# Performance work log

Hardware: AMD Instinct MI355X
Metric: run time of the kernel (lower is better)

Reference implementation:

```python
import jax, jax.numpy as jnp
import numpy as np

NUM_CLASSES = 3
DICE_W, FOCAL_W, CONTR_W = 1.0, 1.0, 0.1
GAMMA, ALPHA = 2.0, 0.25
TEMP = 0.1
SCALE_WEIGHTS = (1.0, 0.8, 0.6)
SMOOTH = 1e-5


def setup_inputs() -> dict:
    key = jax.random.key(0)
    ks = jax.random.split(key, 7)
    return {
        "pred_maps": jax.random.normal(ks[0], (2, 3, 128, 128, 128), jnp.float32),
        "target": jax.random.randint(ks[1], (2, 128, 128, 128), 0, 3, jnp.int64),
        "fmap0": jax.random.normal(ks[2], (2, 48, 16, 16, 16), jnp.float32),
        "fmap1": jax.random.normal(ks[3], (2, 48, 8, 8, 8), jnp.float32),
        "fmap2": jax.random.normal(ks[4], (2, 48, 4, 4, 4), jnp.float32),
        "logits": jax.random.normal(ks[5], (2, 3), jnp.float32),
        "labels": jax.random.randint(ks[6], (2, 3), 0, 2, jnp.int32),
    }


def _dice_loss(pred, target):
    p = jax.nn.softmax(pred, axis=1)                      # [B,C,H,W,D]
    t = jnp.where(target == -1, 0, target)
    oh = jax.nn.one_hot(t, NUM_CLASSES, axis=1, dtype=p.dtype)  # [B,C,H,W,D]
    inter = (p * oh).sum((2, 3, 4))                       # [B,C]
    union = p.sum((2, 3, 4)) + oh.sum((2, 3, 4))
    dice = (2.0 * inter + SMOOTH) / (union + SMOOTH)      # [B,C]
    return 1.0 - dice[:, 1:].mean()                       # exclude background


def _focal_loss(logits, labels):
    pt = jax.nn.sigmoid(logits)
    pt = jnp.where(labels == 1, pt, 1.0 - pt)
    return (-ALPHA * (1.0 - pt) ** GAMMA * jnp.log(pt + 1e-6)).mean()


def _pair_loss(E, wa, wb, offdiag, positive):
    # E: [B,N,N] exp(sim/T); wa, wb: [B,N] class indicator weights
    W = wa[:, :, None] * wb[:, None, :]
    if offdiag is not None:
        W = W * offdiag
    cnt = W.sum((1, 2))
    mean = (E * W).sum((1, 2)) / jnp.maximum(cnt, 1.0)
    val = -jnp.log(mean + 1e-6) if positive else jnp.log1p(mean)
    return jnp.where(cnt > 0, val, 0.0)                   # [B]


def _scale_loss(feat, mask):
    B, C = feat.shape[:2]
    f = feat.reshape(B, C, -1)                            # [B,C,N]
    norm = jnp.sqrt((f * f).sum(1, keepdims=True))
    f = f / jnp.maximum(norm, 1e-12)                      # F.normalize(dim=1)
    m = mask.reshape(B, -1)                               # [B,N]
    E = jnp.exp(jnp.einsum('bcn,bcm->bnm', f, f) / TEMP)  # [B,N,N]
    N = m.shape[1]
    off = 1.0 - jnp.eye(N, dtype=f.dtype)
    w0 = (m == 0).astype(f.dtype)
    w1 = (m == 1).astype(f.dtype)
    w2 = (m == 2).astype(f.dtype)
    loss = _pair_loss(E, w1, w1, off, True)               # htx positive
    loss += _pair_loss(E, w2, w2, off, True)              # mh positive
    loss += _pair_loss(E, w1, w2, None, False)            # htx vs mh
    loss += _pair_loss(E, w0, w1, None, False)            # bg vs htx
    loss += _pair_loss(E, w0, w2, None, False)            # bg vs mh
    return loss.mean()                                    # batch_loss / B


def _contrastive_loss(fmaps, target):
    H = target.shape[1]
    total = 0.0
    for feat, w in zip(fmaps, SCALE_WEIGHTS):
        s = H // feat.shape[2]                            # exact nearest-downsample stride
        mask = target[:, ::s, ::s, ::s]
        total += w * _scale_loss(feat, mask)
    return total


def reference(pred_maps, target, fmap0, fmap1, fmap2, logits, labels):
    dice = _dice_loss(pred_maps, target)
    focal = _focal_loss(logits, labels)
    contr = _contrastive_loss((fmap0, fmap1, fmap2), target)
    total = DICE_W * dice + FOCAL_W * focal + CONTR_W * contr
    return (total, dice, focal, contr)
```

## Files before the change

kernel.cpp:

```cpp
#include <hip/hip_runtime.h>
#include <math.h>

#define VOX (128*128*128)
#define NCH 48

typedef _Float16 half8 __attribute__((ext_vector_type(8)));
typedef float floatx4 __attribute__((ext_vector_type(4)));

__device__ __forceinline__ float waveSum(float v) {
#pragma unroll
    for (int off = 32; off > 0; off >>= 1) v += __shfl_down(v, off, 64);
    return v;
}


__global__ void zero_ws(int* p) { p[threadIdx.x] = 0; }

__global__ __launch_bounds__(256) void count_kernel(const int* __restrict__ target,
                                                    int* __restrict__ cnt) {
    const int scale = blockIdx.y, b = blockIdx.z, z = scale * 2 + b;
    const int N    = (scale == 0) ? 4096 : (scale == 1) ? 512 : 64;
    const int Npad = (scale == 0) ? 4096 : (scale == 1) ? 512 : 128;
    const int n = blockIdx.x * blockDim.x + threadIdx.x;
    int myK = -1;
    if (n < N) {
        const int d = (scale == 0) ? 16 : (scale == 1) ? 8 : 4;
        const int s = 128 / d;
        int i3 = n % d, i2 = (n / d) % d, i1 = n / (d * d);
        myK = target[(size_t)b * VOX + (size_t)(i1 * s) * 16384 + (i2 * s) * 128 + (i3 * s)];
    } else if (n < Npad) {
        myK = 3;
    }
    const int lane = threadIdx.x & 63;
#pragma unroll
    for (int k = 0; k < 4; k++) {
        unsigned long long mb = __ballot(myK == k);
        if (mb && lane == (__ffsll((unsigned long long)mb) - 1))
            atomicAdd(&cnt[z * 4 + k], (int)__popcll(mb));
    }
}

__global__ __launch_bounds__(256) void dice_kernel(const float* __restrict__ pred,
                                                   const int* __restrict__ target,
                                                   float* __restrict__ dice_stage) {
    const int b = blockIdx.z;
    const float4* p0 = (const float4*)(pred + (size_t)b * 3 * VOX);
    const float4* p1 = (const float4*)(pred + (size_t)b * 3 * VOX + VOX);
    const float4* p2 = (const float4*)(pred + (size_t)b * 3 * VOX + 2 * VOX);
    const int4*   tg = (const int4*)(target + (size_t)b * VOX);

    float vals[6] = {0, 0, 0, 0, 0, 0};
    const int V4 = VOX / 4;
    const int stride = gridDim.x * blockDim.x;
    for (int v = blockIdx.x * blockDim.x + threadIdx.x; v < V4; v += stride) {
        float4 a = p0[v], bq = p1[v], cq = p2[v];
        int4 t = tg[v];
        float xs[4][3] = {{a.x, bq.x, cq.x}, {a.y, bq.y, cq.y},
                          {a.z, bq.z, cq.z}, {a.w, bq.w, cq.w}};
        int ts[4] = {t.x, t.y, t.z, t.w};
#pragma unroll
        for (int e = 0; e < 4; e++) {
            float e0 = __expf(xs[e][0]), e1 = __expf(xs[e][1]), e2 = __expf(xs[e][2]);
            float inv = 1.0f / (e0 + e1 + e2);
            float q1 = e1 * inv, q2 = e2 * inv;
            vals[2] += q1;
            vals[3] += q2;
            int tt = ts[e];
            vals[0] += (tt == 1) ? q1 : 0.0f;
            vals[1] += (tt == 2) ? q2 : 0.0f;
            vals[4] += (tt == 1) ? 1.0f : 0.0f;
            vals[5] += (tt == 2) ? 1.0f : 0.0f;
        }
    }
    __shared__ float red[4][6];
    int lane = threadIdx.x & 63, wid = threadIdx.x >> 6;
#pragma unroll
    for (int k = 0; k < 6; k++) {
        float s = waveSum(vals[k]);
        if (lane == 0) red[wid][k] = s;
    }
    __syncthreads();
    if (threadIdx.x < 6) {
        float s = red[0][threadIdx.x] + red[1][threadIdx.x] +
                  red[2][threadIdx.x] + red[3][threadIdx.x];
        dice_stage[(size_t)(b * 512 + blockIdx.x) * 8 + threadIdx.x] = s;
    }
}

__global__ __launch_bounds__(256) void norm_scatter(const float* __restrict__ f0in,
                                                    const float* __restrict__ f1in,
                                                    const float* __restrict__ f2in,
                                                    const int* __restrict__ target,
                                                    _Float16* __restrict__ Fh0,
                                                    _Float16* __restrict__ Fh1,
                                                    _Float16* __restrict__ Fh2,
                                                    const int* __restrict__ cnt,
                                                    int* __restrict__ cursor) {
    const int scale = blockIdx.y, b = blockIdx.z, z = scale * 2 + b;
    const int N    = (scale == 0) ? 4096 : (scale == 1) ? 512 : 64;
    const int Npad = (scale == 0) ? 4096 : (scale == 1) ? 512 : 128;
    const int n = blockIdx.x * blockDim.x + threadIdx.x;
    const int lane = threadIdx.x & 63;

    const int c0 = cnt[z * 4 + 0], c1 = cnt[z * 4 + 1], c2 = cnt[z * 4 + 2];
    const int bases[4] = {0, c0, c0 + c1, c0 + c1 + c2};

    int myK = -1;
    float v[NCH];
    float inv = 0.0f;
    if (n < N) {
        const float* fi = ((scale == 0) ? f0in : (scale == 1) ? f1in : f2in)
                          + (size_t)b * NCH * N + n;
        float ss = 0.0f;
#pragma unroll
        for (int c = 0; c < NCH; c++) { v[c] = fi[(size_t)c * N]; ss += v[c] * v[c]; }
        inv = 1.0f / fmaxf(sqrtf(ss), 1e-12f);
        const int d = (scale == 0) ? 16 : (scale == 1) ? 8 : 4;
        const int s = 128 / d;
        int i3 = n % d, i2 = (n / d) % d, i1 = n / (d * d);
        myK = target[(size_t)b * VOX + (size_t)(i1 * s) * 16384 + (i2 * s) * 128 + (i3 * s)];
    } else if (n < Npad) {
        myK = 3;
#pragma unroll
        for (int c = 0; c < NCH; c++) v[c] = 0.0f;
    }

    int dest = -1;
#pragma unroll
    for (int k = 0; k < 4; k++) {
        unsigned long long mb = __ballot(myK == k);
        int base = 0;
        if (mb) {
            int leader = __ffsll((unsigned long long)mb) - 1;
            if (lane == leader)
                base = atomicAdd(&cursor[z * 4 + k], (int)__popcll(mb));
            base = __shfl(base, leader, 64);
            if (myK == k) {
                int pos = (int)__popcll(mb & ((1ull << lane) - 1ull));
                dest = bases[k] + base + pos;
            }
        }
    }

    if (myK >= 0) {
        _Float16* fo = ((scale == 0) ? Fh0 : (scale == 1) ? Fh1 : Fh2)
                       + (size_t)b * Npad * 64 + (size_t)dest * 64;
#pragma unroll
        for (int g = 0; g < 8; g++) {
            half8 h;
#pragma unroll
            for (int e = 0; e < 8; e++) {
                int c = g * 8 + e;
                h[e] = (c < NCH) ? (_Float16)(v[c] * inv) : (_Float16)0.0f;
            }
            *(half8*)(fo + g * 8) = h;
        }
    }
}

__global__ __launch_bounds__(256) void pair_mfma(const _Float16* __restrict__ Fh0,
                                                 const _Float16* __restrict__ Fh1,
                                                 const _Float16* __restrict__ Fh2,
                                                 const int* __restrict__ cnt,
                                                 float* __restrict__ pair_stage) {
    const int bid = blockIdx.x;
    int z, t;
    if (bid < 1056)      { z = bid / 528; t = bid % 528; }
    else if (bid < 1076) { int i = bid - 1056; z = 2 + i / 10; t = i % 10; }
    else                 { z = 4 + (bid - 1076); t = 0; }

    const int scale = z >> 1, b = z & 1;
    const int Npad = (scale == 0) ? 4096 : (scale == 1) ? 512 : 128;
    const _Float16* F = ((scale == 0) ? Fh0 : (scale == 1) ? Fh1 : Fh2)
                        + (size_t)b * Npad * 64;
    const int B1 = cnt[z * 4 + 0];
    const int B2 = B1 + cnt[z * 4 + 1];
    const int B3 = B2 + cnt[z * 4 + 2];

    int by = (int)((sqrtf(8.0f * (float)t + 1.0f) - 1.0f) * 0.5f);
    while ((by + 1) * (by + 2) / 2 <= t) by++;
    while (by * (by + 1) / 2 > t) by--;
    int bx = t - by * (by + 1) / 2;

    const int tid = threadIdx.x, lane = tid & 63, w = tid >> 6;
    const int wi = w >> 1, wj = w & 1;
    const int m = lane & 15, q = lane >> 4;
    const int ib = bx * 128 + wi * 64, jb = by * 128 + wj * 64;

    float s[5] = {0, 0, 0, 0, 0};

    const bool diag = (ib == jb);
    const bool below = (ib > jb);
    int ciL = (ib >= B1) + (ib >= B2) + (ib >= B3);
    int ciH = (ib + 63 >= B1) + (ib + 63 >= B2) + (ib + 63 >= B3);
    int cjL = (jb >= B1) + (jb >= B2) + (jb >= B3);
    int cjH = (jb + 63 >= B1) + (jb + 63 >= B2) + (jb + 63 >= B3);
    const bool pure = (ciL == ciH) && (cjL == cjH) && !diag;
    int bucket = -1;
    float mult = 1.0f;
    if (pure) {
        int ci = ciL, cj = cjL;
        if (ci == 1 && cj == 1) { bucket = 0; mult = 2.0f; }
        else if (ci == 2 && cj == 2) { bucket = 1; mult = 2.0f; }
        else if (ci == 1 && cj == 2) bucket = 2;
        else if (ci == 0 && cj == 1) bucket = 3;
        else if (ci == 0 && cj == 2) bucket = 4;
    }
    const bool skip = below || (pure && bucket < 0);

    if (!skip) {
        const _Float16* Ai = F + (size_t)(ib + m) * 64 + q * 8;
        const _Float16* Bj = F + (size_t)(jb + m) * 64 + q * 8;

        floatx4 acc_[4][4] = {};
#pragma unroll
        for (int k = 0; k < 2; k++) {
            half8 aF[4], bF[4];
#pragma unroll
            for (int t4 = 0; t4 < 4; t4++) {
                aF[t4] = *(const half8*)(Ai + t4 * 16 * 64 + k * 32);
                bF[t4] = *(const half8*)(Bj + t4 * 16 * 64 + k * 32);
            }
#pragma unroll
            for (int ti = 0; ti < 4; ti++)
#pragma unroll
                for (int tj = 0; tj < 4; tj++)
                    acc_[ti][tj] = __builtin_amdgcn_mfma_f32_16x16x32_f16(
                        aF[ti], bF[tj], acc_[ti][tj], 0, 0, 0);
        }

        if (pure) {
            float ps[4] = {0, 0, 0, 0};
#pragma unroll
            for (int ti = 0; ti < 4; ti++)
#pragma unroll
                for (int tj = 0; tj < 4; tj++)
#pragma unroll
                    for (int r = 0; r < 4; r++)
                        ps[r] += __expf(acc_[ti][tj][r] * 10.0f);
            s[bucket] = ((ps[0] + ps[1]) + (ps[2] + ps[3])) * mult;
        } else {
#pragma unroll
            for (int ti = 0; ti < 4; ti++) {
#pragma unroll
                for (int tj = 0; tj < 4; tj++) {
#pragma unroll
                    for (int r = 0; r < 4; r++) {
                        int gi = ib + ti * 16 + q * 4 + r;
                        int gj = jb + tj * 16 + m;
                        float e = __expf(acc_[ti][tj][r] * 10.0f);
                        bool ok = !diag || (gi < gj);
                        int ci = (gi >= B1) + (gi >= B2) + (gi >= B3);
                        int cj = (gj >= B1) + (gj >= B2) + (gj >= B3);
                        s[0] += (ok && ci == 1 && cj == 1) ? e + e : 0.0f;
                        s[1] += (ok && ci == 2 && cj == 2) ? e + e : 0.0f;
                        s[2] += (ok && ci == 1 && cj == 2) ? e : 0.0f;
                        s[3] += (ok && ci == 0 && cj == 1) ? e : 0.0f;
                        s[4] += (ok && ci == 0 && cj == 2) ? e : 0.0f;
                    }
                }
            }
        }
    }

    __shared__ float red[4][5];
#pragma unroll
    for (int k = 0; k < 5; k++) {
        float r = waveSum(s[k]);
        if (lane == 0) red[w][k] = r;
    }
    __syncthreads();
    if (tid < 5) {
        float r = red[0][tid] + red[1][tid] + red[2][tid] + red[3][tid];
        pair_stage[(size_t)bid * 8 + tid] = r;
    }
}

__global__ __launch_bounds__(1024) void reduce_finalize(const float* __restrict__ dice_stage,
                                                        const int* __restrict__ cnt,
                                                        const float* __restrict__ pair_stage,
                                                        const float* __restrict__ logits,
                                                        const int* __restrict__ labels,
                                                        float* __restrict__ out) {
    __shared__ float D[2][6], S[6][5];
    const int tid = threadIdx.x, w = tid >> 6, lane = tid & 63;

    if (w < 2) {
        float v[6] = {0, 0, 0, 0, 0, 0};
#pragma unroll
        for (int i = 0; i < 8; i++) {
            const float* row = dice_stage + (size_t)(w * 512 + i * 64 + lane) * 8;
#pragma unroll
            for (int k = 0; k < 6; k++) v[k] += row[k];
        }
#pragma unroll
        for (int k = 0; k < 6; k++) {
            float r = waveSum(v[k]);
            if (lane == 0) D[w][k] = r;
        }
    } else if (w < 8) {
        int z = w - 2;
        int start = (z == 0) ? 0 : (z == 1) ? 528 : (z == 2) ? 1056
                    : (z == 3) ? 1066 : (z == 4) ? 1076 : 1077;
        int n = (z < 2) ? 528 : (z < 4) ? 10 : 1;
        float v[5] = {0, 0, 0, 0, 0};
        for (int i = lane; i < n; i += 64) {
            const float* row = pair_stage + (size_t)(start + i) * 8;
#pragma unroll
            for (int k = 0; k < 5; k++) v[k] += row[k];
        }
#pragma unroll
        for (int k = 0; k < 5; k++) {
            float r = waveSum(v[k]);
            if (lane == 0) S[z][k] = r;
        }
    }
    __syncthreads();
    if (tid != 0) return;

    float dsum = 0.0f;
    for (int b = 0; b < 2; b++)
        for (int c = 0; c < 2; c++)
            dsum += (2.0f * D[b][c] + 1e-5f) / (D[b][2 + c] + D[b][4 + c] + 1e-5f);
    float dice = 1.0f - dsum * 0.25f;

    float fsum = 0.0f;
    for (int i = 0; i < 6; i++) {
        float x = logits[i];
        float pt = 1.0f / (1.0f + __expf(-x));
        if (labels[i] != 1) pt = 1.0f - pt;
        fsum += -0.25f * (1.0f - pt) * (1.0f - pt) * logf(pt + 1e-6f);
    }
    float focal = fsum * (1.0f / 6.0f);

    const float sw[3] = {1.0f, 0.8f, 0.6f};
    float contr = 0.0f;
    for (int sc = 0; sc < 3; sc++) {
        float bsum = 0.0f;
        for (int b = 0; b < 2; b++) {
            int z = sc * 2 + b;
            float S11 = S[z][0], S22 = S[z][1], S12 = S[z][2],
                  S01 = S[z][3], S02 = S[z][4];
            float c0 = (float)cnt[z * 4 + 0], c1 = (float)cnt[z * 4 + 1],
                  c2 = (float)cnt[z * 4 + 2];
            float l = 0.0f, c, mean;
            c = c1 * c1 - c1; mean = S11 / fmaxf(c, 1.0f);
            l += (c > 0.0f) ? -logf(mean + 1e-6f) : 0.0f;
            c = c2 * c2 - c2; mean = S22 / fmaxf(c, 1.0f);
            l += (c > 0.0f) ? -logf(mean + 1e-6f) : 0.0f;
            c = c1 * c2; mean = S12 / fmaxf(c, 1.0f);
            l += (c > 0.0f) ? log1pf(mean) : 0.0f;
            c = c0 * c1; mean = S01 / fmaxf(c, 1.0f);
            l += (c > 0.0f) ? log1pf(mean) : 0.0f;
            c = c0 * c2; mean = S02 / fmaxf(c, 1.0f);
            l += (c > 0.0f) ? log1pf(mean) : 0.0f;
            bsum += l;
        }
        contr += sw[sc] * bsum * 0.5f;
    }
    float total = dice + focal + 0.1f * contr;
    out[0] = total;
    out[1] = dice;
    out[2] = focal;
    out[3] = contr;
}

extern "C" void kernel_launch(void* const* d_in, const int* in_sizes, int n_in,
                              void* d_out, int out_size, void* d_ws, size_t ws_size,
                              hipStream_t stream) {
    const float* pred   = (const float*)d_in[0];
    const int*   target = (const int*)d_in[1];
    const float* f0     = (const float*)d_in[2];
    const float* f1     = (const float*)d_in[3];
    const float* f2     = (const float*)d_in[4];
    const float* logits = (const float*)d_in[5];
    const int*   labels = (const int*)d_in[6];
    float* out = (float*)d_out;

    char* ws = (char*)d_ws;
    int*   cnt        = (int*)ws;
    int*   cursor     = (int*)(ws + 128);
    float* dice_stage = (float*)(ws + 4096);
    float* pair_stage = (float*)(ws + 36864);
    _Float16* Fh0 = (_Float16*)(ws + 131072);
    _Float16* Fh1 = (_Float16*)(ws + 1179648);
    _Float16* Fh2 = (_Float16*)(ws + 1310720);

    zero_ws<<<dim3(1), dim3(64), 0, stream>>>(cnt);
    count_kernel<<<dim3(16, 3, 2), dim3(256), 0, stream>>>(target, cnt);
    dice_kernel<<<dim3(512, 1, 2), dim3(256), 0, stream>>>(pred, target, dice_stage);
    norm_scatter<<<dim3(16, 3, 2), dim3(256), 0, stream>>>(f0, f1, f2, target,
                                                           Fh0, Fh1, Fh2, cnt, cursor);
    pair_mfma<<<dim3(1078), dim3(256), 0, stream>>>(Fh0, Fh1, Fh2, cnt, pair_stage);
    reduce_finalize<<<dim3(1), dim3(1024), 0, stream>>>(dice_stage, cnt, pair_stage,
                                                        logits, labels, out);
}
```

Measured before the change: 152.7 us.

## Fuse count and scatter into one block-per-scale sort, halve pair grid

Replaces the zero, count and scatter kernels with a single norm_sort kernel that uses one 1024-thread block per (scale, batch). It counts classes and computes scatter offsets in shared memory, removing two launches and the global atomics. The pair kernel now processes two triangular tiles per block for the large scales, halving the grid and the staging rows that the finalize kernel reads. The cost is that norm_sort runs only 6 blocks, which serialises the 4096-point normalisation over a few CUs and may become a latency bottleneck.

```diff
diff --git a/kernel.cpp b/kernel.cpp
--- a/kernel.cpp
+++ b/kernel.cpp
@@ -13,32 +13,6 @@
     return v;
 }
 
-
-__global__ void zero_ws(int* p) { p[threadIdx.x] = 0; }
-
-__global__ __launch_bounds__(256) void count_kernel(const int* __restrict__ target,
-                                                    int* __restrict__ cnt) {
-    const int scale = blockIdx.y, b = blockIdx.z, z = scale * 2 + b;
-    const int N    = (scale == 0) ? 4096 : (scale == 1) ? 512 : 64;
-    const int Npad = (scale == 0) ? 4096 : (scale == 1) ? 512 : 128;
-    const int n = blockIdx.x * blockDim.x + threadIdx.x;
-    int myK = -1;
-    if (n < N) {
-        const int d = (scale == 0) ? 16 : (scale == 1) ? 8 : 4;
-        const int s = 128 / d;
-        int i3 = n % d, i2 = (n / d) % d, i1 = n / (d * d);
-        myK = target[(size_t)b * VOX + (size_t)(i1 * s) * 16384 + (i2 * s) * 128 + (i3 * s)];
-    } else if (n < Npad) {
-        myK = 3;
-    }
-    const int lane = threadIdx.x & 63;
-#pragma unroll
-    for (int k = 0; k < 4; k++) {
-        unsigned long long mb = __ballot(myK == k);
-        if (mb && lane == (__ffsll((unsigned long long)mb) - 1))
-            atomicAdd(&cnt[z * 4 + k], (int)__popcll(mb));
-    }
-}
 
 __global__ __launch_bounds__(256) void dice_kernel(const float* __restrict__ pred,
                                                    const int* __restrict__ target,
@@ -87,64 +61,83 @@
     }
 }
 
-__global__ __launch_bounds__(256) void norm_scatter(const float* __restrict__ f0in,
-                                                    const float* __restrict__ f1in,
-                                                    const float* __restrict__ f2in,
-                                                    const int* __restrict__ target,
-                                                    _Float16* __restrict__ Fh0,
-                                                    _Float16* __restrict__ Fh1,
-                                                    _Float16* __restrict__ Fh2,
-                                                    const int* __restrict__ cnt,
-                                                    int* __restrict__ cursor) {
-    const int scale = blockIdx.y, b = blockIdx.z, z = scale * 2 + b;
+__global__ __launch_bounds__(1024) void norm_sort(const float* __restrict__ f0in,
+                                                  const float* __restrict__ f1in,
+                                                  const float* __restrict__ f2in,
+                                                  const int* __restrict__ target,
+                                                  _Float16* __restrict__ Fh0,
+                                                  _Float16* __restrict__ Fh1,
+                                                  _Float16* __restrict__ Fh2,
+                                                  int* __restrict__ cnt) {
+    const int z = blockIdx.x, scale = z >> 1, b = z & 1;
     const int N    = (scale == 0) ? 4096 : (scale == 1) ? 512 : 64;
     const int Npad = (scale == 0) ? 4096 : (scale == 1) ? 512 : 128;
-    const int n = blockIdx.x * blockDim.x + threadIdx.x;
-    const int lane = threadIdx.x & 63;
-
-    const int c0 = cnt[z * 4 + 0], c1 = cnt[z * 4 + 1], c2 = cnt[z * 4 + 2];
-    const int bases[4] = {0, c0, c0 + c1, c0 + c1 + c2};
-
-    int myK = -1;
-    float v[NCH];
-    float inv = 0.0f;
-    if (n < N) {
-        const float* fi = ((scale == 0) ? f0in : (scale == 1) ? f1in : f2in)
-                          + (size_t)b * NCH * N + n;
-        float ss = 0.0f;
-#pragma unroll
-        for (int c = 0; c < NCH; c++) { v[c] = fi[(size_t)c * N]; ss += v[c] * v[c]; }
-        inv = 1.0f / fmaxf(sqrtf(ss), 1e-12f);
-        const int d = (scale == 0) ? 16 : (scale == 1) ? 8 : 4;
-        const int s = 128 / d;
-        int i3 = n % d, i2 = (n / d) % d, i1 = n / (d * d);
-        myK = target[(size_t)b * VOX + (size_t)(i1 * s) * 16384 + (i2 * s) * 128 + (i3 * s)];
-    } else if (n < Npad) {
-        myK = 3;
-#pragma unroll
-        for (int c = 0; c < NCH; c++) v[c] = 0.0f;
-    }
-
-    int dest = -1;
-#pragma unroll
-    for (int k = 0; k < 4; k++) {
-        unsigned long long mb = __ballot(myK == k);
-        int base = 0;
-        if (mb) {
-            int leader = __ffsll((unsigned long long)mb) - 1;
-            if (lane == leader)
-                base = atomicAdd(&cursor[z * 4 + k], (int)__popcll(mb));
-            base = __shfl(base, leader, 64);
-            if (myK == k) {
-                int pos = (int)__popcll(mb & ((1ull << lane) - 1ull));
-                dest = bases[k] + base + pos;
+    const int d    = (scale == 0) ? 16 : (scale == 1) ? 8 : 4;
+    const int s    = 128 / d;
+    const float* fin = (scale == 0) ? f0in : (scale == 1) ? f1in : f2in;
+    _Float16* fout   = (scale == 0) ? Fh0 : (scale == 1) ? Fh1 : Fh2;
+
+    __shared__ int clsLds[4096];
+    __shared__ int cCnt[4], cCur[4], base[4];
+    const int tid = threadIdx.x, lane = tid & 63;
+    if (tid < 4) { cCnt[tid] = 0; cCur[tid] = 0; }
+    __syncthreads();
+
+    for (int n = tid; n < Npad; n += 1024) {
+        int k = 3;
+        if (n < N) {
+            int i3 = n % d, i2 = (n / d) % d, i1 = n / (d * d);
+            k = target[(size_t)b * VOX + (size_t)(i1 * s) * 16384 + (i2 * s) * 128 + (i3 * s)];
+        }
+        clsLds[n] = k;
+#pragma unroll
+        for (int kk = 0; kk < 4; kk++) {
+            unsigned long long mb = __ballot(k == kk);
+            if (mb && lane == (__ffsll((unsigned long long)mb) - 1))
+                atomicAdd(&cCnt[kk], (int)__popcll(mb));
+        }
+    }
+    __syncthreads();
+    if (tid == 0) {
+        base[0] = 0;
+        base[1] = cCnt[0];
+        base[2] = cCnt[0] + cCnt[1];
+        base[3] = cCnt[0] + cCnt[1] + cCnt[2];
+        cnt[z * 4 + 0] = cCnt[0];
+        cnt[z * 4 + 1] = cCnt[1];
+        cnt[z * 4 + 2] = cCnt[2];
+        cnt[z * 4 + 3] = cCnt[3];
+    }
+    __syncthreads();
+
+    for (int n = tid; n < Npad; n += 1024) {
+        int k = clsLds[n];
+        int dest = 0;
+#pragma unroll
+        for (int kk = 0; kk < 4; kk++) {
+            unsigned long long mb = __ballot(k == kk);
+            if (mb) {
+                int leader = __ffsll((unsigned long long)mb) - 1;
+                int boff = 0;
+                if (lane == leader) boff = atomicAdd(&cCur[kk], (int)__popcll(mb));
+                boff = __shfl(boff, leader, 64);
+                if (k == kk)
+                    dest = base[kk] + boff + (int)__popcll(mb & ((1ull << lane) - 1ull));
             }
         }
-    }
-
-    if (myK >= 0) {
-        _Float16* fo = ((scale == 0) ? Fh0 : (scale == 1) ? Fh1 : Fh2)
-                       + (size_t)b * Npad * 64 + (size_t)dest * 64;
+        float v[NCH];
+        float inv = 0.0f;
+        if (n < N) {
+            const float* fi = fin + (size_t)b * NCH * N + n;
+            float ss = 0.0f;
+#pragma unroll
+            for (int c = 0; c < NCH; c++) { v[c] = fi[(size_t)c * N]; ss += v[c] * v[c]; }
+            inv = 1.0f / fmaxf(sqrtf(ss), 1e-12f);
+        } else {
+#pragma unroll
+            for (int c = 0; c < NCH; c++) v[c] = 0.0f;
+        }
+        _Float16* fo = fout + (size_t)b * Npad * 64 + (size_t)dest * 64;
 #pragma unroll
         for (int g = 0; g < 8; g++) {
             half8 h;
@@ -164,10 +157,10 @@
                                                  const int* __restrict__ cnt,
                                                  float* __restrict__ pair_stage) {
     const int bid = blockIdx.x;
-    int z, t;
-    if (bid < 1056)      { z = bid / 528; t = bid % 528; }
-    else if (bid < 1076) { int i = bid - 1056; z = 2 + i / 10; t = i % 10; }
-    else                 { z = 4 + (bid - 1076); t = 0; }
+    int z, t0, nt, tstep;
+    if (bid < 528)      { z = bid / 264; t0 = bid % 264; nt = 2; tstep = 264; }
+    else if (bid < 548) { int i = bid - 528; z = 2 + i / 10; t0 = i % 10; nt = 1; tstep = 0; }
+    else                { z = 4 + (bid - 548); t0 = 0; nt = 1; tstep = 0; }
 
     const int scale = z >> 1, b = z & 1;
     const int Npad = (scale == 0) ? 4096 : (scale == 1) ? 512 : 128;
@@ -177,38 +170,40 @@
     const int B2 = B1 + cnt[z * 4 + 1];
     const int B3 = B2 + cnt[z * 4 + 2];
 
-    int by = (int)((sqrtf(8.0f * (float)t + 1.0f) - 1.0f) * 0.5f);
-    while ((by + 1) * (by + 2) / 2 <= t) by++;
-    while (by * (by + 1) / 2 > t) by--;
-    int bx = t - by * (by + 1) / 2;
-
     const int tid = threadIdx.x, lane = tid & 63, w = tid >> 6;
     const int wi = w >> 1, wj = w & 1;
     const int m = lane & 15, q = lane >> 4;
-    const int ib = bx * 128 + wi * 64, jb = by * 128 + wj * 64;
 
     float s[5] = {0, 0, 0, 0, 0};
 
-    const bool diag = (ib == jb);
-    const bool below = (ib > jb);
-    int ciL = (ib >= B1) + (ib >= B2) + (ib >= B3);
-    int ciH = (ib + 63 >= B1) + (ib + 63 >= B2) + (ib + 63 >= B3);
-    int cjL = (jb >= B1) + (jb >= B2) + (jb >= B3);
-    int cjH = (jb + 63 >= B1) + (jb + 63 >= B2) + (jb + 63 >= B3);
-    const bool pure = (ciL == ciH) && (cjL == cjH) && !diag;
-    int bucket = -1;
-    float mult = 1.0f;
-    if (pure) {
-        int ci = ciL, cj = cjL;
-        if (ci == 1 && cj == 1) { bucket = 0; mult = 2.0f; }
-        else if (ci == 2 && cj == 2) { bucket = 1; mult = 2.0f; }
-        else if (ci == 1 && cj == 2) bucket = 2;
-        else if (ci == 0 && cj == 1) bucket = 3;
-        else if (ci == 0 && cj == 2) bucket = 4;
-    }
-    const bool skip = below || (pure && bucket < 0);
-
-    if (!skip) {
+    for (int it = 0; it < nt; it++) {
+        int t = t0 + it * tstep;
+        int by = (int)((sqrtf(8.0f * (float)t + 1.0f) - 1.0f) * 0.5f);
+        while ((by + 1) * (by + 2) / 2 <= t) by++;
+        while (by * (by + 1) / 2 > t) by--;
+        int bx = t - by * (by + 1) / 2;
+
+        const int ib = bx * 128 + wi * 64, jb = by * 128 + wj * 64;
+
+        const bool diag = (ib == jb);
+        const bool below = (ib > jb);
+        int ciL = (ib >= B1) + (ib >= B2) + (ib >= B3);
+        int ciH = (ib + 63 >= B1) + (ib + 63 >= B2) + (ib + 63 >= B3);
+        int cjL = (jb >= B1) + (jb >= B2) + (jb >= B3);
+        int cjH = (jb + 63 >= B1) + (jb + 63 >= B2) + (jb + 63 >= B3);
+        const bool pure = (ciL == ciH) && (cjL == cjH) && !diag;
+        int bucket = -1;
+        float mult = 1.0f;
+        if (pure) {
+            int ci = ciL, cj = cjL;
+            if (ci == 1 && cj == 1) { bucket = 0; mult = 2.0f; }
+            else if (ci == 2 && cj == 2) { bucket = 1; mult = 2.0f; }
+            else if (ci == 1 && cj == 2) bucket = 2;
+            else if (ci == 0 && cj == 1) bucket = 3;
+            else if (ci == 0 && cj == 2) bucket = 4;
+        }
+        if (below || (pure && bucket < 0)) continue;
+
         const _Float16* Ai = F + (size_t)(ib + m) * 64 + q * 8;
         const _Float16* Bj = F + (size_t)(jb + m) * 64 + q * 8;
 
@@ -238,7 +233,7 @@
 #pragma unroll
                     for (int r = 0; r < 4; r++)
                         ps[r] += __expf(acc_[ti][tj][r] * 10.0f);
-            s[bucket] = ((ps[0] + ps[1]) + (ps[2] + ps[3])) * mult;
+            s[bucket] += ((ps[0] + ps[1]) + (ps[2] + ps[3])) * mult;
         } else {
 #pragma unroll
             for (int ti = 0; ti < 4; ti++) {
@@ -276,12 +271,12 @@
     }
 }
 
-__global__ __launch_bounds__(1024) void reduce_finalize(const float* __restrict__ dice_stage,
-                                                        const int* __restrict__ cnt,
-                                                        const float* __restrict__ pair_stage,
-                                                        const float* __restrict__ logits,
-                                                        const int* __restrict__ labels,
-                                                        float* __restrict__ out) {
+__global__ __launch_bounds__(512) void reduce_finalize(const float* __restrict__ dice_stage,
+                                                       const int* __restrict__ cnt,
+                                                       const float* __restrict__ pair_stage,
+                                                       const float* __restrict__ logits,
+                                                       const int* __restrict__ labels,
+                                                       float* __restrict__ out) {
     __shared__ float D[2][6], S[6][5];
     const int tid = threadIdx.x, w = tid >> 6, lane = tid & 63;
 
@@ -298,11 +293,11 @@
             float r = waveSum(v[k]);
             if (lane == 0) D[w][k] = r;
         }
-    } else if (w < 8) {
+    } else {
         int z = w - 2;
-        int start = (z == 0) ? 0 : (z == 1) ? 528 : (z == 2) ? 1056
-                    : (z == 3) ? 1066 : (z == 4) ? 1076 : 1077;
-        int n = (z < 2) ? 528 : (z < 4) ? 10 : 1;
+        int start = (z == 0) ? 0 : (z == 1) ? 264 : (z == 2) ? 528
+                    : (z == 3) ? 538 : (z == 4) ? 548 : 549;
+        int n = (z < 2) ? 264 : (z < 4) ? 10 : 1;
         float v[5] = {0, 0, 0, 0, 0};
         for (int i = lane; i < n; i += 64) {
             const float* row = pair_stage + (size_t)(start + i) * 8;
@@ -379,19 +374,16 @@
 
     char* ws = (char*)d_ws;
     int*   cnt        = (int*)ws;
-    int*   cursor     = (int*)(ws + 128);
     float* dice_stage = (float*)(ws + 4096);
     float* pair_stage = (float*)(ws + 36864);
     _Float16* Fh0 = (_Float16*)(ws + 131072);
     _Float16* Fh1 = (_Float16*)(ws + 1179648);
     _Float16* Fh2 = (_Float16*)(ws + 1310720);
 
-    zero_ws<<<dim3(1), dim3(64), 0, stream>>>(cnt);
-    count_kernel<<<dim3(16, 3, 2), dim3(256), 0, stream>>>(target, cnt);
     dice_kernel<<<dim3(512, 1, 2), dim3(256), 0, stream>>>(pred, target, dice_stage);
-    norm_scatter<<<dim3(16, 3, 2), dim3(256), 0, stream>>>(f0, f1, f2, target,
-                                                           Fh0, Fh1, Fh2, cnt, cursor);
-    pair_mfma<<<dim3(1078), dim3(256), 0, stream>>>(Fh0, Fh1, Fh2, cnt, pair_stage);
-    reduce_finalize<<<dim3(1), dim3(1024), 0, stream>>>(dice_stage, cnt, pair_stage,
-                                                        logits, labels, out);
-}
+    norm_sort<<<dim3(6), dim3(1024), 0, stream>>>(f0, f1, f2, target,
+                                                  Fh0, Fh1, Fh2, cnt);
+    pair_mfma<<<dim3(550), dim3(256), 0, stream>>>(Fh0, Fh1, Fh2, cnt, pair_stage);
+    reduce_finalize<<<dim3(1), dim3(512), 0, stream>>>(dice_stage, cnt, pair_stage,
+                                                       logits, labels, out);
+}
```

After: 170.2 us. 1.11x slower.
